# Kernel optimization log

Measured on AMD Instinct MI355X. Metric: run time of the kernel, lower is better.

The kernel has to match this reference:

```python
import jax, jax.numpy as jnp
import numpy as np

N_U, N_I, D = 8192, 8192, 128


def setup_inputs() -> dict:
    key = jax.random.key(0)
    k1, k2, k3, k4, k5 = jax.random.split(key, 5)
    h_u = jax.random.normal(k1, (N_U, D), dtype=jnp.float32)
    h_i = jax.random.normal(k2, (N_I, D), dtype=jnp.float32)
    ui_adj = jax.random.randint(k3, (N_U, N_I), 0, 2).astype(jnp.int32)
    # learned params: W is nn.Linear(d, d, bias=False) -> weight [d, d]; a is [2d]
    W = jax.random.normal(k4, (D, D), dtype=jnp.float32) * (1.0 / np.sqrt(D))
    a = jax.random.normal(k5, (2 * D,), dtype=jnp.float32) * 0.1
    return {"h_u": h_u, "h_i": h_i, "ui_adj": ui_adj, "W": W, "a": a}


def reference(h_u, h_i, ui_adj, W, a):
    # torch nn.Linear: x @ W.T
    Wu = h_u @ W.T                      # [N_u, d]
    Wi = h_i @ W.T                      # [N_i, d]
    d = Wu.shape[1]
    a1 = Wu @ a[:d]                     # [N_u]
    a2 = Wi @ a[d:]                     # [N_i]
    e = jax.nn.leaky_relu(a1[:, None] + a2[None, :], negative_slope=0.2)  # [N_u, N_i]
    adj = ui_adj != 0
    no_item = ~adj.any(axis=-1)         # rows with zero neighbors
    e = jnp.where(adj, e, -jnp.inf)
    # avoid all -inf rows (torch softmax -> NaN -> nan_to_num -> 0); use 0 logits then zero alpha
    e = jnp.where(no_item[:, None], 0.0, e)
    alpha = jax.nn.softmax(e, axis=-1)  # [N_u, N_i]
    alpha = jnp.where(no_item[:, None], 0.0, alpha)
    out = alpha @ Wi                    # [N_u, d]
    out = jnp.where(no_item[:, None], 0.0, out)
    return (out, alpha)
```

## Files before the change

### kernel.cpp

```cpp
#include <hip/hip_runtime.h>

#define NU 8192
#define NI 8192
#define DD 128

typedef float fx4 __attribute__((ext_vector_type(4)));
typedef int   ix4 __attribute__((ext_vector_type(4)));
typedef short bx8 __attribute__((ext_vector_type(8)));
typedef short sx4 __attribute__((ext_vector_type(4)));

__device__ __forceinline__ short f2bf(float f) {
  unsigned u = __float_as_uint(f);
  u = (u + 0x7FFFu + ((u >> 16) & 1u)) >> 16;
  return (short)u;
}
__device__ __forceinline__ float lrelu(float x) { return fmaxf(x, 0.2f * x); }

__global__ __launch_bounds__(256) void k_prep(
    const float* __restrict__ hU, const float* __restrict__ hI,
    const float* __restrict__ W, const float* __restrict__ a,
    float* __restrict__ a1, float* __restrict__ e1, float* __restrict__ e2,
    short* __restrict__ WiT, float* __restrict__ blkmax)
{
  __shared__ float Wl[128 * 128];
  __shared__ float vv[2][128];
  __shared__ float red[64];
  const int tid = threadIdx.x;
#pragma unroll
  for (int it = 0; it < 16; ++it) {
    int idx = it * 1024 + tid * 4;
    *(fx4*)(Wl + idx) = *(const fx4*)(W + idx);
  }
  __syncthreads();
  if (tid < 128) {
    float s1 = 0.f, s2 = 0.f;
    for (int k = 0; k < DD; ++k) {
      float w = Wl[k * 128 + tid];
      s1 += a[k] * w;
      s2 += a[DD + k] * w;
    }
    vv[0][tid] = s1; vv[1][tid] = s2;
  }
  __syncthreads();

  const int i0 = blockIdx.x * 64;
  {
    const int rg = tid & 15;
    const int kg = tid >> 4;
    const int r0 = i0 + rg * 4;
    const int k0 = kg * 8;
    float acc[4][8];
#pragma unroll
    for (int r = 0; r < 4; ++r)
#pragma unroll
      for (int c = 0; c < 8; ++c) acc[r][c] = 0.f;
    for (int j = 0; j < 128; j += 4) {
      fx4 wv8[8], hv[4];
#pragma unroll
      for (int c = 0; c < 8; ++c) wv8[c] = *(const fx4*)(Wl + (k0 + c) * 128 + j);
#pragma unroll
      for (int r = 0; r < 4; ++r) hv[r] = *(const fx4*)(hI + (size_t)(r0 + r) * DD + j);
#pragma unroll
      for (int r = 0; r < 4; ++r)
#pragma unroll
        for (int c = 0; c < 8; ++c)
          acc[r][c] += hv[r][0]*wv8[c][0] + hv[r][1]*wv8[c][1] + hv[r][2]*wv8[c][2] + hv[r][3]*wv8[c][3];
    }
#pragma unroll
    for (int c = 0; c < 8; ++c) {
      sx4 pk;
#pragma unroll
      for (int r = 0; r < 4; ++r) pk[r] = f2bf(acc[r][c]);
      *(sx4*)(WiT + (size_t)(k0 + c) * NI + r0) = pk;
    }
  }

  if (tid < 64) {
    const int row = i0 + tid;
    const fx4* hv = (const fx4*)(hU + (size_t)row * DD);
    const fx4* vq = (const fx4*)&vv[0][0];
    float s = 0.f;
#pragma unroll
    for (int q = 0; q < DD / 4; ++q) {
      fx4 hq = hv[q], vqq = vq[q];
      s += hq[0]*vqq[0] + hq[1]*vqq[1] + hq[2]*vqq[2] + hq[3]*vqq[3];
    }
    a1[row] = s;
  } else if (tid < 128) {
    const int row = i0 + (tid - 64);
    const fx4* hv = (const fx4*)(hI + (size_t)row * DD);
    const fx4* vq = (const fx4*)&vv[1][0];
    float s = 0.f;
#pragma unroll
    for (int q = 0; q < DD / 4; ++q) {
      fx4 hq = hv[q], vqq = vq[q];
      s += hq[0]*vqq[0] + hq[1]*vqq[1] + hq[2]*vqq[2] + hq[3]*vqq[3];
    }
    e1[row] = __expf(s);
    e2[row] = __expf(0.2f * s);
    red[tid - 64] = s;
  }
  __syncthreads();
  if (tid < 32) red[tid] = fmaxf(red[tid], red[tid + 32]);
  __syncthreads();
  if (tid < 16) red[tid] = fmaxf(red[tid], red[tid + 16]);
  __syncthreads();
  if (tid < 8)  red[tid] = fmaxf(red[tid], red[tid + 8]);
  __syncthreads();
  if (tid < 4)  red[tid] = fmaxf(red[tid], red[tid + 4]);
  __syncthreads();
  if (tid == 0)
    blkmax[blockIdx.x] = fmaxf(fmaxf(red[0], red[1]), fmaxf(red[2], red[3]));
}

__global__ void k_mx(const float* __restrict__ blkmax, float* __restrict__ mx) {
  __shared__ float r[128];
  const int tid = threadIdx.x;
  r[tid] = blkmax[tid];
  __syncthreads();
  for (int s = 64; s > 0; s >>= 1) {
    if (tid < s) r[tid] = fmaxf(r[tid], r[tid + s]);
    __syncthreads();
  }
  if (tid == 0) mx[0] = r[0];
}

__global__ __launch_bounds__(512, 4) void k_fuseA(
    const int* __restrict__ adj, const float* __restrict__ a1g,
    const float* __restrict__ e1g, const float* __restrict__ e2g,
    const float* __restrict__ mxp,
    fx4* __restrict__ kcons, unsigned* __restrict__ mask,
    float* __restrict__ alphap)
{
  const int row  = blockIdx.x;
  const int tid  = threadIdx.x;
  const int lane = tid & 63;
  const int wv   = tid >> 6;
  const size_t base = (size_t)row * NI;
  ix4 m[4];
#pragma unroll
  for (int q = 0; q < 4; ++q)
    m[q] = __builtin_nontemporal_load((const ix4*)(adj + base + q * 2048 + tid * 4));
  const float A  = a1g[row];
  const float C  = lrelu(A + mxp[0]);
  const float K1 = __expf(A - C);
  const float K2 = __expf(0.2f * A - C);
  const float T1 = __expf(-A);
  fx4 p[4];
  float ps = 0.f;
#pragma unroll
  for (int q = 0; q < 4; ++q) {
    const int i0 = q * 2048 + tid * 4;
    const fx4 E1 = *(const fx4*)(e1g + i0);
    const fx4 E2 = *(const fx4*)(e2g + i0);
    unsigned long long b[4];
#pragma unroll
    for (int e = 0; e < 4; ++e) {
      const bool mm  = (m[q][e] != 0);
      const bool sel = (E1[e] > T1);
      const float val = sel ? E1[e] * K1 : E2[e] * K2;
      const float pv  = mm ? val : 0.f;
      p[q][e] = pv;
      ps += pv;
      b[e] = __ballot(mm);
    }
    if (lane < 8) {
      unsigned w = 0u;
#pragma unroll
      for (int e = 0; e < 4; ++e) {
        unsigned x = (unsigned)((b[e] >> (lane * 8)) & 0xFFull);
        x = (x | (x << 12)) & 0x000F000Fu;
        x = (x | (x << 6))  & 0x03030303u;
        x = (x | (x << 3))  & 0x11111111u;
        w |= x << e;
      }
      mask[(size_t)row * 256 + q * 64 + wv * 8 + lane] = w;
    }
  }
#pragma unroll
  for (int st = 1; st < 64; st <<= 1) ps += __shfl_xor(ps, st, 64);
  __shared__ float lp[8];
  if (lane == 0) lp[wv] = ps;
  __syncthreads();
  const float l  = ((lp[0] + lp[1]) + (lp[2] + lp[3]))
                 + ((lp[4] + lp[5]) + (lp[6] + lp[7]));
  const float ri = (l > 0.f) ? (1.f / l) : 0.f;
#pragma unroll
  for (int q = 0; q < 4; ++q) {
    fx4 o;
#pragma unroll
    for (int e = 0; e < 4; ++e) o[e] = p[q][e] * ri;
    __builtin_nontemporal_store(o, (fx4*)(alphap + base + q * 2048 + tid * 4));
  }
  if (tid == 0) kcons[row] = (fx4){K1 * ri, K2 * ri, T1, ri};
}

__global__ __launch_bounds__(512, 4) void k_gemm(
    const unsigned* __restrict__ mask, const fx4* __restrict__ kcons,
    const float* __restrict__ e1g, const float* __restrict__ e2g,
    const short* __restrict__ WiT, float* __restrict__ partial)
{
  __shared__ __align__(16) char lds[32768];
  const int tid  = threadIdx.x;
  const int lane = tid & 63;
  const int wv   = tid >> 6;
  const int wm   = wv & 3;
  const int kk   = wv >> 2;
  const int uTile = (int)blockIdx.x >> 2;
  const int quar  = (int)blockIdx.x & 3;
  const int u0 = uTile * 64;
  const int ib = quar * 2048;
  const int lr = lane & 15, lg = lane >> 4;

  const int rowm = u0 + wm * 16 + lr;
  const fx4 kcm = kcons[rowm];
  const float K1m = kcm[0], K2m = kcm[1], T1m = kcm[2];
  const unsigned* mrow = mask + (size_t)rowm * 256 + quar * 64;

  const int sd = tid >> 3;
  const int si = tid & 7;
  const short* g0 = WiT + (size_t)sd * NI + ib + si * 8;
  const short* g1 = WiT + (size_t)(sd + 64) * NI + ib + si * 8;
  const int swz = (si * 16) ^ ((sd & 7) << 4);
  const int w0 = sd * 128 + swz;
  const int w1 = (sd + 64) * 128 + swz;

  fx4 acc[8];
#pragma unroll
  for (int n = 0; n < 8; ++n) acc[n] = (fx4){0.f, 0.f, 0.f, 0.f};

  bx8 sA = *(const bx8*)g0;
  bx8 sB = *(const bx8*)g1;
  *(bx8*)(lds + w0) = sA;
  *(bx8*)(lds + w1) = sB;

  for (int c = 0; c < 32; ++c) {
    char* buf = lds + (c & 1) * 16384;
    const int nxt = ((c + 1) & 1) * 16384;
    if (c < 31) {
      sA = *(const bx8*)(g0 + (c + 1) * 64);
      sB = *(const bx8*)(g1 + (c + 1) * 64);
    }
    __syncthreads();

    {
      const int ksg = c * 2 + kk;
      const unsigned by = (mrow[ksg] >> (lg * 8)) & 0xFFu;
      const int io = ksg * 32 + lg * 8;
      const fx4 e1a = *(const fx4*)(e1g + ib + io);
      const fx4 e1b = *(const fx4*)(e1g + ib + io + 4);
      const fx4 e2a = *(const fx4*)(e2g + ib + io);
      const fx4 e2b = *(const fx4*)(e2g + ib + io + 4);
      bx8 af;
#pragma unroll
      for (int j = 0; j < 8; ++j) {
        const float e1v = (j < 4) ? e1a[j] : e1b[j - 4];
        const float e2v = (j < 4) ? e2a[j] : e2b[j - 4];
        const float val = (e1v > T1m) ? e1v * K1m : e2v * K2m;
        af[j] = ((by >> j) & 1u) ? f2bf(val) : (short)0;
      }
#pragma unroll
      for (int nf = 0; nf < 8; ++nf) {
        const int d = nf * 16 + lr;
        const bx8 bf = *(const bx8*)(buf + d * 128 +
                        ((kk * 64 + lg * 16) ^ ((lr & 7) << 4)));
        acc[nf] = __builtin_amdgcn_mfma_f32_16x16x32_bf16(af, bf, acc[nf], 0, 0, 0);
      }
    }

    if (c < 31) {
      *(bx8*)(lds + nxt + w0) = sA;
      *(bx8*)(lds + nxt + w1) = sB;
    }
  }

  __syncthreads();
  float* red = (float*)lds;
  if (kk == 0) {
#pragma unroll
    for (int nf = 0; nf < 8; ++nf)
#pragma unroll
      for (int v = 0; v < 4; ++v)
        red[(wm * 16 + lg * 4 + v) * 128 + nf * 16 + lr] = acc[nf][v];
  }
  __syncthreads();
  if (kk == 1) {
    float* pb = partial + (size_t)blockIdx.x * (64 * 128);
#pragma unroll
    for (int nf = 0; nf < 8; ++nf)
#pragma unroll
      for (int v = 0; v < 4; ++v) {
        const int idx = (wm * 16 + lg * 4 + v) * 128 + nf * 16 + lr;
        pb[idx] = red[idx] + acc[nf][v];
      }
  }
}

__global__ __launch_bounds__(512) void k_comb(
    const float* __restrict__ partial, float* __restrict__ outp)
{
  const int g = blockIdx.x * 512 + threadIdx.x;
  const int u = g >> 5;
  const int c4 = (g & 31) * 4;
  const int uTile = u >> 6, r = u & 63;
  const float* p0 = partial + ((size_t)uTile * 4) * 8192 + r * 128 + c4;
  fx4 s = *(const fx4*)p0;
#pragma unroll
  for (int q = 1; q < 4; ++q) {
    fx4 t = *(const fx4*)(p0 + (size_t)q * 8192);
    s[0] += t[0]; s[1] += t[1]; s[2] += t[2]; s[3] += t[3];
  }
  *(fx4*)(outp + (size_t)u * DD + c4) = s;
}

extern "C" void kernel_launch(void* const* d_in, const int* in_sizes, int n_in,
                              void* d_out, int out_size, void* d_ws, size_t ws_size,
                              hipStream_t stream) {
  (void)in_sizes; (void)n_in; (void)out_size; (void)ws_size;
  const float* h_u = (const float*)d_in[0];
  const float* h_i = (const float*)d_in[1];
  const int*   adj = (const int*)d_in[2];
  const float* W   = (const float*)d_in[3];
  const float* a   = (const float*)d_in[4];

  float* outp   = (float*)d_out;
  float* alphap = (float*)d_out + (size_t)NU * DD;

  char* ws = (char*)d_ws;
  float*    mx     = (float*)(ws + 1024);
  float*    blkmax = (float*)(ws + 2048);
  float*    a1     = (float*)(ws + 4096);
  float*    e1t    = (float*)(ws + 102400);
  float*    e2t    = (float*)(ws + 135168);
  short*    WiT    = (short*)(ws + 262144);
  unsigned* mask   = (unsigned*)(ws + 2359296);
  float*    part   = (float*)(ws + 11534336);
  fx4*      kcons  = (fx4*)(ws + 29360128);

  k_prep  <<<128,  256, 0, stream>>>(h_u, h_i, W, a, a1, e1t, e2t, WiT, blkmax);
  k_mx    <<<1,    128, 0, stream>>>(blkmax, mx);
  k_fuseA <<<NU,   512, 0, stream>>>(adj, a1, e1t, e2t, mx, kcons, mask, alphap);
  k_gemm  <<<512,  512, 0, stream>>>(mask, kcons, e1t, e2t, WiT, part);
  k_comb  <<<512,  512, 0, stream>>>(part, outp);
}
```

Measured before the change: 177.1 us.

## Spread prep over more blocks and fold global max reduction into attention kernel

```diff
diff --git a/kernel.cpp b/kernel.cpp
--- a/kernel.cpp
+++ b/kernel.cpp
@@ -24,7 +24,7 @@
 {
   __shared__ float Wl[128 * 128];
   __shared__ float vv[2][128];
-  __shared__ float red[64];
+  __shared__ float red[16];
   const int tid = threadIdx.x;
 #pragma unroll
   for (int it = 0; it < 16; ++it) {
@@ -43,39 +43,31 @@
   }
   __syncthreads();
 
-  const int i0 = blockIdx.x * 64;
+  const int i0 = blockIdx.x * 16;
+
   {
     const int rg = tid & 15;
     const int kg = tid >> 4;
-    const int r0 = i0 + rg * 4;
+    const int r0 = i0 + rg;
     const int k0 = kg * 8;
-    float acc[4][8];
-#pragma unroll
-    for (int r = 0; r < 4; ++r)
-#pragma unroll
-      for (int c = 0; c < 8; ++c) acc[r][c] = 0.f;
+    float acc[8];
+#pragma unroll
+    for (int c = 0; c < 8; ++c) acc[c] = 0.f;
     for (int j = 0; j < 128; j += 4) {
-      fx4 wv8[8], hv[4];
+      fx4 wv8[8];
 #pragma unroll
       for (int c = 0; c < 8; ++c) wv8[c] = *(const fx4*)(Wl + (k0 + c) * 128 + j);
-#pragma unroll
-      for (int r = 0; r < 4; ++r) hv[r] = *(const fx4*)(hI + (size_t)(r0 + r) * DD + j);
-#pragma unroll
-      for (int r = 0; r < 4; ++r)
-#pragma unroll
-        for (int c = 0; c < 8; ++c)
-          acc[r][c] += hv[r][0]*wv8[c][0] + hv[r][1]*wv8[c][1] + hv[r][2]*wv8[c][2] + hv[r][3]*wv8[c][3];
-    }
-#pragma unroll
-    for (int c = 0; c < 8; ++c) {
-      sx4 pk;
-#pragma unroll
-      for (int r = 0; r < 4; ++r) pk[r] = f2bf(acc[r][c]);
-      *(sx4*)(WiT + (size_t)(k0 + c) * NI + r0) = pk;
-    }
-  }
-
-  if (tid < 64) {
+      const fx4 hv = *(const fx4*)(hI + (size_t)r0 * DD + j);
+#pragma unroll
+      for (int c = 0; c < 8; ++c)
+        acc[c] += hv[0]*wv8[c][0] + hv[1]*wv8[c][1] + hv[2]*wv8[c][2] + hv[3]*wv8[c][3];
+    }
+#pragma unroll
+    for (int c = 0; c < 8; ++c)
+      WiT[(size_t)(k0 + c) * NI + r0] = f2bf(acc[c]);
+  }
+
+  if (tid < 16) {
     const int row = i0 + tid;
     const fx4* hv = (const fx4*)(hU + (size_t)row * DD);
     const fx4* vq = (const fx4*)&vv[0][0];
@@ -86,7 +78,7 @@
       s += hq[0]*vqq[0] + hq[1]*vqq[1] + hq[2]*vqq[2] + hq[3]*vqq[3];
     }
     a1[row] = s;
-  } else if (tid < 128) {
+  } else if (tid >= 64 && tid < 80) {
     const int row = i0 + (tid - 64);
     const fx4* hv = (const fx4*)(hI + (size_t)row * DD);
     const fx4* vq = (const fx4*)&vv[1][0];
@@ -101,34 +93,18 @@
     red[tid - 64] = s;
   }
   __syncthreads();
-  if (tid < 32) red[tid] = fmaxf(red[tid], red[tid + 32]);
-  __syncthreads();
-  if (tid < 16) red[tid] = fmaxf(red[tid], red[tid + 16]);
-  __syncthreads();
-  if (tid < 8)  red[tid] = fmaxf(red[tid], red[tid + 8]);
-  __syncthreads();
-  if (tid < 4)  red[tid] = fmaxf(red[tid], red[tid + 4]);
-  __syncthreads();
-  if (tid == 0)
-    blkmax[blockIdx.x] = fmaxf(fmaxf(red[0], red[1]), fmaxf(red[2], red[3]));
-}
-
-__global__ void k_mx(const float* __restrict__ blkmax, float* __restrict__ mx) {
-  __shared__ float r[128];
-  const int tid = threadIdx.x;
-  r[tid] = blkmax[tid];
-  __syncthreads();
-  for (int s = 64; s > 0; s >>= 1) {
-    if (tid < s) r[tid] = fmaxf(r[tid], r[tid + s]);
-    __syncthreads();
-  }
-  if (tid == 0) mx[0] = r[0];
+  if (tid == 0) {
+    float m = red[0];
+#pragma unroll
+    for (int k = 1; k < 16; ++k) m = fmaxf(m, red[k]);
+    blkmax[blockIdx.x] = m;
+  }
 }
 
 __global__ __launch_bounds__(512, 4) void k_fuseA(
     const int* __restrict__ adj, const float* __restrict__ a1g,
     const float* __restrict__ e1g, const float* __restrict__ e2g,
-    const float* __restrict__ mxp,
+    const float* __restrict__ blkmax,
     fx4* __restrict__ kcons, unsigned* __restrict__ mask,
     float* __restrict__ alphap)
 {
@@ -141,8 +117,22 @@
 #pragma unroll
   for (int q = 0; q < 4; ++q)
     m[q] = __builtin_nontemporal_load((const ix4*)(adj + base + q * 2048 + tid * 4));
+
+  __shared__ float smax[8];
+  __shared__ float lp[8];
+  {
+    float bm = blkmax[tid];
+#pragma unroll
+    for (int st = 1; st < 64; st <<= 1) bm = fmaxf(bm, __shfl_xor(bm, st, 64));
+    if (lane == 0) smax[wv] = bm;
+  }
+  __syncthreads();
+  float mA2 = smax[0];
+#pragma unroll
+  for (int w = 1; w < 8; ++w) mA2 = fmaxf(mA2, smax[w]);
+
   const float A  = a1g[row];
-  const float C  = lrelu(A + mxp[0]);
+  const float C  = lrelu(A + mA2);
   const float K1 = __expf(A - C);
   const float K2 = __expf(0.2f * A - C);
   const float T1 = __expf(-A);
@@ -179,7 +169,6 @@
   }
 #pragma unroll
   for (int st = 1; st < 64; st <<= 1) ps += __shfl_xor(ps, st, 64);
-  __shared__ float lp[8];
   if (lane == 0) lp[wv] = ps;
   __syncthreads();
   const float l  = ((lp[0] + lp[1]) + (lp[2] + lp[3]))
@@ -327,7 +316,6 @@
   float* alphap = (float*)d_out + (size_t)NU * DD;
 
   char* ws = (char*)d_ws;
-  float*    mx     = (float*)(ws + 1024);
   float*    blkmax = (float*)(ws + 2048);
   float*    a1     = (float*)(ws + 4096);
   float*    e1t    = (float*)(ws + 102400);
@@ -337,9 +325,8 @@
   float*    part   = (float*)(ws + 11534336);
   fx4*      kcons  = (fx4*)(ws + 29360128);
 
-  k_prep  <<<128,  256, 0, stream>>>(h_u, h_i, W, a, a1, e1t, e2t, WiT, blkmax);
-  k_mx    <<<1,    128, 0, stream>>>(blkmax, mx);
-  k_fuseA <<<NU,   512, 0, stream>>>(adj, a1, e1t, e2t, mx, kcons, mask, alphap);
+  k_prep  <<<512,  256, 0, stream>>>(h_u, h_i, W, a, a1, e1t, e2t, WiT, blkmax);
+  k_fuseA <<<NU,   512, 0, stream>>>(adj, a1, e1t, e2t, blkmax, kcons, mask, alphap);
   k_gemm  <<<512,  512, 0, stream>>>(mask, kcons, e1t, e2t, WiT, part);
   k_comb  <<<512,  512, 0, stream>>>(part, outp);
 }
```

New measurement: 166.9 us, median of 2. 1.06x faster.
